# Kernel tuning notes

Hardware: AMD Instinct MI355X
Metric: run time of the kernel (lower is better)

Reference implementation:

```python
import jax, jax.numpy as jnp
import numpy as np

B, S, D, H = 4, 1024, 1024, 16
DH = D // H  # head dim = 64
NEG = 1e9  # keras Softmax masking constant for fp32


def setup_inputs() -> dict:
    key = jax.random.key(0)
    ks = jax.random.split(key, 7)
    return {
        "inputs": jax.random.normal(ks[0], (B, S, D), jnp.float32),
        "mask": jax.random.randint(ks[1], (B, 1, 1, S), 0, 2) > 0,
        "interaction": jax.random.normal(ks[2], (B, S, S, H), jnp.float32) * 0.1,
        "W_Q": jax.random.normal(ks[3], (D, D), jnp.float32) * 0.02,
        "W_K": jax.random.normal(ks[4], (D, D), jnp.float32) * 0.02,
        "W_V": jax.random.normal(ks[5], (D, D), jnp.float32) * 0.02,
        "W_O": jax.random.normal(ks[6], (D, D), jnp.float32) * 0.02,
    }


def reference(inputs, mask, interaction, W_Q, W_K, W_V, W_O):
    b, s, d = inputs.shape
    def proj(W):
        # [B,S,D] @ [D,D] -> [B,S,H,DH] -> [B,H,S,DH]
        return (inputs @ W).reshape(b, s, H, DH).transpose(0, 2, 1, 3)
    Q, K, V = proj(W_Q), proj(W_K), proj(W_V)
    scores = jnp.einsum("bhqd,bhkd->bhqk", Q, K) / (DH ** 0.5)
    # interaction [B,S,S,H] -> [B,H,S,S], additive bias before softmax
    scores = scores + interaction.transpose(0, 3, 1, 2)
    # keras Softmax(mask=...): add -1e9 where mask is False, softmax over last axis
    scores = jnp.where(mask, scores, scores - NEG)
    attn = jax.nn.softmax(scores, axis=-1)
    hidden = jnp.einsum("bhqk,bhkd->bhqd", attn, V)
    hidden = hidden.transpose(0, 2, 1, 3).reshape(b, s, d)
    return hidden @ W_O
```

## Files before the change

### kernel.cpp

```cpp
#include <hip/hip_runtime.h>
#include <hip/hip_bf16.h>
#include <stdint.h>

#define BDIM 4
#define SDIM 1024
#define DDIM 1024
#define HDIM 16
#define DHDIM 64

typedef __bf16 bf16_t;
typedef __bf16 bf16x8 __attribute__((ext_vector_type(8)));
typedef __bf16 bf16x4 __attribute__((ext_vector_type(4)));
typedef float f32x4 __attribute__((ext_vector_type(4)));

typedef __attribute__((address_space(3))) uint32_t lds_u32;
typedef const __attribute__((address_space(1))) uint32_t glb_u32;

__device__ __forceinline__ void glds16(const void* g, void* l) {
    __builtin_amdgcn_global_load_lds((glb_u32*)g, (lds_u32*)l, 16, 0, 0);
}


__global__ __launch_bounds__(256) void convert_x_kernel(const float* __restrict__ X,
                                                        bf16_t* __restrict__ Xb, int n) {
    int i = (blockIdx.x * 256 + threadIdx.x) * 4;
    if (i >= n) return;
    float4 v = *(const float4*)(X + i);
    bf16x4 o;
    o[0] = (bf16_t)v.x; o[1] = (bf16_t)v.y; o[2] = (bf16_t)v.z; o[3] = (bf16_t)v.w;
    *(bf16x4*)(Xb + i) = o;
}

__global__ __launch_bounds__(256) void transpose_w_kernel(const float* __restrict__ W0,
                                                          const float* __restrict__ W1,
                                                          const float* __restrict__ W2,
                                                          const float* __restrict__ W3,
                                                          bf16_t* __restrict__ Wt) {
    __shared__ float tile[32][33];
    int z = blockIdx.z;
    const float* W = (z == 0) ? W0 : (z == 1) ? W1 : (z == 2) ? W2 : W3;
    bf16_t* dst = Wt + (size_t)z * DDIM * DDIM;
    int bx = blockIdx.x * 32;
    int by = blockIdx.y * 32;
    int x = threadIdx.x & 31, y0 = threadIdx.x >> 5;
#pragma unroll
    for (int i = 0; i < 4; i++) {
        int y = y0 + i * 8;
        tile[y][x] = W[(size_t)(by + y) * DDIM + bx + x];
    }
    __syncthreads();
#pragma unroll
    for (int i = 0; i < 4; i++) {
        int y = y0 + i * 8;
        dst[(size_t)(bx + y) * DDIM + by + x] = (bf16_t)tile[x][y];
    }
}

__global__ __launch_bounds__(1024) void mask_flag_kernel(const unsigned char* __restrict__ mb,
                                                         int* __restrict__ flag) {
    __shared__ int any;
    if (threadIdx.x == 0) any = 0;
    __syncthreads();
    int loc = 0;
    for (int i = threadIdx.x; i < BDIM * SDIM; i += 1024)
        if ((i & 3) && mb[i]) loc = 1;
    if (loc) any = 1;
    __syncthreads();
    if (threadIdx.x == 0) *flag = any ? 1 : 0;
}

template <int MODE>
__global__ __launch_bounds__(256) void gemm_bt_kernel(const bf16_t* __restrict__ A,
                                                      const bf16_t* __restrict__ Bt,
                                                      bf16_t* __restrict__ Qo, bf16_t* __restrict__ Ko,
                                                      bf16_t* __restrict__ Vto, float* __restrict__ Co) {
    __shared__ bf16_t As[128 * 32];
    __shared__ bf16_t Bs[128 * 32];
    const int m0 = blockIdx.x * 128;
    const int n0 = blockIdx.y * 128;
    const int t = threadIdx.x;
    const int lane = t & 63, w = t >> 6;
    const int wm = w & 1, wn = w >> 1;
    const int low = lane & 15, quad = lane >> 4;
    f32x4 acc[4][4] = {};

    const int srow = w * 16 + (lane >> 2);
    const int koff = (lane & 3) * 8;
    const bf16_t* Ag = A + (size_t)(m0 + srow) * DDIM + koff;
    const bf16_t* Bg = Bt + (size_t)(n0 + srow) * DDIM + koff;
    bf16_t* AsW = As + w * 512;
    bf16_t* BsW = Bs + w * 512;

    for (int k0 = 0; k0 < DDIM; k0 += 32) {
        __syncthreads();
        glds16(Ag + k0, AsW);
        glds16(Ag + (size_t)64 * DDIM + k0, AsW + 64 * 32);
        glds16(Bg + k0, BsW);
        glds16(Bg + (size_t)64 * DDIM + k0, BsW + 64 * 32);
        __syncthreads();
        bf16x8 af[4], bv[4];
#pragma unroll
        for (int mt = 0; mt < 4; mt++)
            af[mt] = *(const bf16x8*)(As + (wm * 64 + mt * 16 + low) * 32 + quad * 8);
#pragma unroll
        for (int nt = 0; nt < 4; nt++)
            bv[nt] = *(const bf16x8*)(Bs + (wn * 64 + nt * 16 + low) * 32 + quad * 8);
#pragma unroll
        for (int mt = 0; mt < 4; mt++)
#pragma unroll
            for (int nt = 0; nt < 4; nt++)
                acc[mt][nt] = __builtin_amdgcn_mfma_f32_16x16x32_bf16(af[mt], bv[nt], acc[mt][nt], 0, 0, 0);
    }

#pragma unroll
    for (int mt = 0; mt < 4; mt++) {
#pragma unroll
        for (int nt = 0; nt < 4; nt++) {
#pragma unroll
            for (int r = 0; r < 4; r++) {
                int mrow = m0 + wm * 64 + mt * 16 + quad * 4 + r;
                int ncol = n0 + wn * 64 + nt * 16 + low;
                float vv = acc[mt][nt][r];
                if (MODE == 0) {
                    int which = ncol >> 10, nl = ncol & 1023;
                    int h = nl >> 6, dh = nl & 63;
                    int b = mrow >> 10, s = mrow & 1023;
                    if (which == 0)
                        Qo[((size_t)(b * HDIM + h) * SDIM + s) * DHDIM + dh] = (bf16_t)(vv * 0.125f);
                    else if (which == 1)
                        Ko[((size_t)(b * HDIM + h) * SDIM + s) * DHDIM + dh] = (bf16_t)vv;
                    else
                        Vto[((size_t)(b * HDIM + h) * DHDIM + dh) * SDIM + s] = (bf16_t)vv;
                } else {
                    Co[(size_t)mrow * DDIM + ncol] = vv;
                }
            }
        }
    }
}

__global__ __launch_bounds__(512) void attn_kernel(const bf16_t* __restrict__ Q,
                                                   const bf16_t* __restrict__ K,
                                                   const bf16_t* __restrict__ Vt,
                                                   const float* __restrict__ inter,
                                                   const unsigned char* __restrict__ maskb,
                                                   const int* __restrict__ flagp,
                                                   bf16_t* __restrict__ hid) {
    constexpr int KS = 20;
    constexpr int HS = 64 * KS + 4;
    __shared__ bf16_t bias_l[16 * HS];
    __shared__ float pen_l[SDIM];
    __shared__ bf16_t P[8][16 * 72];
    const int b = blockIdx.y;
    const int q0 = blockIdx.x * 16;
    const int t = threadIdx.x;
    const int w = t >> 6, lane = t & 63;
    const int low = lane & 15, quad = lane >> 4;
    const int h0 = w * 2;
    const int mstride = (*flagp) ? 1 : 4;

    for (int k = t; k < SDIM; k += 512)
        pen_l[k] = maskb[((size_t)b * SDIM + k) * mstride] ? 0.f : 1.0e9f;

    bf16x8 qf[2][2];
#pragma unroll
    for (int hh = 0; hh < 2; hh++) {
        const bf16_t* Qb = Q + ((size_t)(b * HDIM + h0 + hh) * SDIM + q0) * DHDIM;
        qf[hh][0] = *(const bf16x8*)(Qb + low * DHDIM + quad * 8);
        qf[hh][1] = *(const bf16x8*)(Qb + low * DHDIM + 32 + quad * 8);
    }

    const int sq = t >> 5;
    const int so = (t & 31) * 4;
    const int hb = (t & 3) * 4;
    const int kb = (t & 31) >> 2;
    const float* srcQ = inter + ((size_t)(b * SDIM + q0 + sq) * SDIM) * HDIM + so;

    float4 regs[8];
#pragma unroll
    for (int i = 0; i < 8; i++) regs[i] = *(const float4*)(srcQ + i * 128);

    float mrow[2][4], lrow[2][4];
    f32x4 accO[2][4] = {};
#pragma unroll
    for (int hh = 0; hh < 2; hh++)
#pragma unroll
        for (int r = 0; r < 4; r++) { mrow[hh][r] = -3.0e38f; lrow[hh][r] = 0.f; }

    __syncthreads();

    for (int c = 0; c < SDIM / 64; c++) {
#pragma unroll
        for (int i = 0; i < 8; i++) {
            int kl = kb + i * 8;
            float p = pen_l[c * 64 + kl];
            float4 v = regs[i];
            bf16_t* d = bias_l + kl * KS + sq;
            d[(hb + 0) * HS] = (bf16_t)(v.x - p);
            d[(hb + 1) * HS] = (bf16_t)(v.y - p);
            d[(hb + 2) * HS] = (bf16_t)(v.z - p);
            d[(hb + 3) * HS] = (bf16_t)(v.w - p);
        }
        __syncthreads();
        if (c + 1 < SDIM / 64) {
#pragma unroll
            for (int i = 0; i < 8; i++)
                regs[i] = *(const float4*)(srcQ + (c + 1) * 1024 + i * 128);
        }
        const int kbase = c * 64;
#pragma unroll
        for (int hh = 0; hh < 2; hh++) {
            const int h = h0 + hh;
            const bf16_t* Kb = K + (size_t)(b * HDIM + h) * SDIM * DHDIM;
            const bf16_t* VtB = Vt + (size_t)(b * HDIM + h) * DHDIM * SDIM;
            f32x4 sacc[4];
#pragma unroll
            for (int nt = 0; nt < 4; nt++) {
                const bf16_t* kp = Kb + (size_t)(kbase + nt * 16 + low) * DHDIM;
                bf16x8 kf0 = *(const bf16x8*)(kp + quad * 8);
                bf16x8 kf1 = *(const bf16x8*)(kp + 32 + quad * 8);
                f32x4 z = {};
                z = __builtin_amdgcn_mfma_f32_16x16x32_bf16(qf[hh][0], kf0, z, 0, 0, 0);
                z = __builtin_amdgcn_mfma_f32_16x16x32_bf16(qf[hh][1], kf1, z, 0, 0, 0);
                sacc[nt] = z;
            }
            float sv[4][4];
#pragma unroll
            for (int nt = 0; nt < 4; nt++) {
                bf16x4 bv = *(const bf16x4*)(bias_l + h * HS + (nt * 16 + low) * KS + quad * 4);
#pragma unroll
                for (int r = 0; r < 4; r++) sv[nt][r] = sacc[nt][r] + (float)bv[r];
            }
#pragma unroll
            for (int r = 0; r < 4; r++) {
                float vmx = fmaxf(fmaxf(sv[0][r], sv[1][r]), fmaxf(sv[2][r], sv[3][r]));
                vmx = fmaxf(vmx, __shfl_xor(vmx, 1));
                vmx = fmaxf(vmx, __shfl_xor(vmx, 2));
                vmx = fmaxf(vmx, __shfl_xor(vmx, 4));
                vmx = fmaxf(vmx, __shfl_xor(vmx, 8));
                float mn = fmaxf(mrow[hh][r], vmx);
                float alpha = __expf(mrow[hh][r] - mn);
                mrow[hh][r] = mn;
                lrow[hh][r] *= alpha;
#pragma unroll
                for (int nt = 0; nt < 4; nt++) accO[hh][nt][r] *= alpha;
                float rs = 0.f;
#pragma unroll
                for (int nt = 0; nt < 4; nt++) {
                    float p = __expf(sv[nt][r] - mn);
                    sv[nt][r] = p;
                    rs += p;
                }
                rs += __shfl_xor(rs, 1);
                rs += __shfl_xor(rs, 2);
                rs += __shfl_xor(rs, 4);
                rs += __shfl_xor(rs, 8);
                lrow[hh][r] += rs;
            }
            bf16_t* Pw = &P[w][0];
#pragma unroll
            for (int nt = 0; nt < 4; nt++)
#pragma unroll
                for (int r = 0; r < 4; r++)
                    Pw[(quad * 4 + r) * 72 + nt * 16 + low] = (bf16_t)sv[nt][r];
#pragma unroll
            for (int step = 0; step < 2; step++) {
                bf16x8 pf = *(const bf16x8*)(Pw + low * 72 + step * 32 + quad * 8);
#pragma unroll
                for (int nt = 0; nt < 4; nt++) {
                    bf16x8 vf = *(const bf16x8*)(VtB + (size_t)(nt * 16 + low) * SDIM +
                                                 kbase + step * 32 + quad * 8);
                    accO[hh][nt] = __builtin_amdgcn_mfma_f32_16x16x32_bf16(pf, vf, accO[hh][nt], 0, 0, 0);
                }
            }
        }
        __syncthreads();
    }
#pragma unroll
    for (int hh = 0; hh < 2; hh++) {
#pragma unroll
        for (int r = 0; r < 4; r++) {
            float inv = 1.f / lrow[hh][r];
#pragma unroll
            for (int nt = 0; nt < 4; nt++) {
                hid[((size_t)b * SDIM + q0 + quad * 4 + r) * DDIM + (h0 + hh) * 64 + nt * 16 + low] =
                    (bf16_t)(accO[hh][nt][r] * inv);
            }
        }
    }
}


extern "C" void kernel_launch(void* const* d_in, const int* in_sizes, int n_in,
                              void* d_out, int out_size, void* d_ws, size_t ws_size,
                              hipStream_t stream) {
    const float* X = (const float*)d_in[0];
    const unsigned char* maskb = (const unsigned char*)d_in[1];
    const float* inter = (const float*)d_in[2];
    const float* WQ = (const float*)d_in[3];
    const float* WK = (const float*)d_in[4];
    const float* WV = (const float*)d_in[5];
    const float* WO = (const float*)d_in[6];
    float* out = (float*)d_out;

    char* ws = (char*)d_ws;
    const size_t MB = 1024 * 1024;
    bf16_t* Xb  = (bf16_t*)(ws + 0 * MB);
    bf16_t* Wt  = (bf16_t*)(ws + 8 * MB);
    bf16_t* Qm  = (bf16_t*)(ws + 16 * MB);
    bf16_t* Km  = (bf16_t*)(ws + 24 * MB);
    bf16_t* Vtm = (bf16_t*)(ws + 32 * MB);
    bf16_t* hid = (bf16_t*)(ws + 40 * MB);
    int* flag   = (int*)(ws + 48 * MB);

    convert_x_kernel<<<BDIM * SDIM * DDIM / (256 * 4), 256, 0, stream>>>(X, Xb, BDIM * SDIM * DDIM);
    transpose_w_kernel<<<dim3(32, 32, 4), 256, 0, stream>>>(WQ, WK, WV, WO, Wt);
    mask_flag_kernel<<<1, 1024, 0, stream>>>(maskb, flag);
    gemm_bt_kernel<0><<<dim3(32, 24), 256, 0, stream>>>(Xb, Wt, Qm, Km, Vtm, nullptr);
    attn_kernel<<<dim3(SDIM / 16, BDIM), 512, 0, stream>>>(Qm, Km, Vtm, inter, maskb, flag, hid);
    gemm_bt_kernel<1><<<dim3(32, 8), 256, 0, stream>>>(hid, Wt + (size_t)3 * DDIM * DDIM,
                                                       nullptr, nullptr, nullptr, out);
}
```

Baseline: 639.2 us.

## Use one wave per head with 32-key chunks and double-buffered bias in attention

The attention kernel goes from 512 to 1024 threads, so each of 16 waves handles a single head instead of two. The key chunk shrinks from 64 to 32, and the interaction bias plus mask penalty is written into a double-buffered LDS tile. The next chunk's bias is loaded and stored after the current chunk's MFMAs, which drops one barrier per iteration and overlaps the bias staging with compute. The mask penalty is now read straight from global memory per chunk instead of from a precomputed LDS array, and launch bounds of (1024,4) may constrain registers.

New measurement: 565.5 us. -11.5%, faster.

```diff
diff --git a/kernel.cpp b/kernel.cpp
--- a/kernel.cpp
+++ b/kernel.cpp
@@ -139,153 +139,139 @@
     }
 }
 
-__global__ __launch_bounds__(512) void attn_kernel(const bf16_t* __restrict__ Q,
-                                                   const bf16_t* __restrict__ K,
-                                                   const bf16_t* __restrict__ Vt,
-                                                   const float* __restrict__ inter,
-                                                   const unsigned char* __restrict__ maskb,
-                                                   const int* __restrict__ flagp,
-                                                   bf16_t* __restrict__ hid) {
+__global__ __launch_bounds__(1024, 4) void attn_kernel(const bf16_t* __restrict__ Q,
+                                                       const bf16_t* __restrict__ K,
+                                                       const bf16_t* __restrict__ Vt,
+                                                       const float* __restrict__ inter,
+                                                       const unsigned char* __restrict__ maskb,
+                                                       const int* __restrict__ flagp,
+                                                       bf16_t* __restrict__ hid) {
     constexpr int KS = 20;
-    constexpr int HS = 64 * KS + 4;
-    __shared__ bf16_t bias_l[16 * HS];
-    __shared__ float pen_l[SDIM];
-    __shared__ bf16_t P[8][16 * 72];
+    constexpr int HS = 32 * KS + 4;
+    __shared__ bf16_t bias_l[2][16 * HS];
+    __shared__ bf16_t P[16][16 * 40];
     const int b = blockIdx.y;
     const int q0 = blockIdx.x * 16;
     const int t = threadIdx.x;
     const int w = t >> 6, lane = t & 63;
     const int low = lane & 15, quad = lane >> 4;
-    const int h0 = w * 2;
+    const int h = w;
     const int mstride = (*flagp) ? 1 : 4;
 
-    for (int k = t; k < SDIM; k += 512)
-        pen_l[k] = maskb[((size_t)b * SDIM + k) * mstride] ? 0.f : 1.0e9f;
-
-    bf16x8 qf[2][2];
-#pragma unroll
-    for (int hh = 0; hh < 2; hh++) {
-        const bf16_t* Qb = Q + ((size_t)(b * HDIM + h0 + hh) * SDIM + q0) * DHDIM;
-        qf[hh][0] = *(const bf16x8*)(Qb + low * DHDIM + quad * 8);
-        qf[hh][1] = *(const bf16x8*)(Qb + low * DHDIM + 32 + quad * 8);
-    }
-
-    const int sq = t >> 5;
-    const int so = (t & 31) * 4;
-    const int hb = (t & 3) * 4;
-    const int kb = (t & 31) >> 2;
-    const float* srcQ = inter + ((size_t)(b * SDIM + q0 + sq) * SDIM) * HDIM + so;
-
-    float4 regs[8];
-#pragma unroll
-    for (int i = 0; i < 8; i++) regs[i] = *(const float4*)(srcQ + i * 128);
-
-    float mrow[2][4], lrow[2][4];
-    f32x4 accO[2][4] = {};
-#pragma unroll
-    for (int hh = 0; hh < 2; hh++)
-#pragma unroll
-        for (int r = 0; r < 4; r++) { mrow[hh][r] = -3.0e38f; lrow[hh][r] = 0.f; }
-
-    __syncthreads();
-
-    for (int c = 0; c < SDIM / 64; c++) {
-#pragma unroll
-        for (int i = 0; i < 8; i++) {
-            int kl = kb + i * 8;
-            float p = pen_l[c * 64 + kl];
-            float4 v = regs[i];
-            bf16_t* d = bias_l + kl * KS + sq;
-            d[(hb + 0) * HS] = (bf16_t)(v.x - p);
-            d[(hb + 1) * HS] = (bf16_t)(v.y - p);
-            d[(hb + 2) * HS] = (bf16_t)(v.z - p);
-            d[(hb + 3) * HS] = (bf16_t)(v.w - p);
-        }
+    const int kl = lane >> 1;
+    const int hb = (lane & 1) * 8;
+    const float* srcQ = inter + ((size_t)(b * SDIM + q0 + w) * SDIM) * HDIM + lane * 8;
+    const unsigned char* mb = maskb + (size_t)b * SDIM * mstride;
+
+    const bf16_t* Qb = Q + ((size_t)(b * HDIM + h) * SDIM + q0) * DHDIM;
+    bf16x8 qf0 = *(const bf16x8*)(Qb + low * DHDIM + quad * 8);
+    bf16x8 qf1 = *(const bf16x8*)(Qb + low * DHDIM + 32 + quad * 8);
+
+    const bf16_t* Kb = K + (size_t)(b * HDIM + h) * SDIM * DHDIM;
+    const bf16_t* VtB = Vt + (size_t)(b * HDIM + h) * DHDIM * SDIM;
+    bf16_t* Pw = &P[w][0];
+
+    float mrow[4], lrow[4];
+    f32x4 accO[4] = {};
+#pragma unroll
+    for (int r = 0; r < 4; r++) { mrow[r] = -3.0e38f; lrow[r] = 0.f; }
+
+    float4 r0 = *(const float4*)(srcQ + 0);
+    float4 r1 = *(const float4*)(srcQ + 4);
+    float pcur = mb[kl * mstride] ? 0.f : 1.0e9f;
+    {
+        bf16_t* d = &bias_l[0][kl * KS + w];
+        d[(hb + 0) * HS] = (bf16_t)(r0.x - pcur);
+        d[(hb + 1) * HS] = (bf16_t)(r0.y - pcur);
+        d[(hb + 2) * HS] = (bf16_t)(r0.z - pcur);
+        d[(hb + 3) * HS] = (bf16_t)(r0.w - pcur);
+        d[(hb + 4) * HS] = (bf16_t)(r1.x - pcur);
+        d[(hb + 5) * HS] = (bf16_t)(r1.y - pcur);
+        d[(hb + 6) * HS] = (bf16_t)(r1.z - pcur);
+        d[(hb + 7) * HS] = (bf16_t)(r1.w - pcur);
+    }
+
+    for (int c = 0; c < SDIM / 32; c++) {
         __syncthreads();
-        if (c + 1 < SDIM / 64) {
-#pragma unroll
-            for (int i = 0; i < 8; i++)
-                regs[i] = *(const float4*)(srcQ + (c + 1) * 1024 + i * 128);
-        }
-        const int kbase = c * 64;
-#pragma unroll
-        for (int hh = 0; hh < 2; hh++) {
-            const int h = h0 + hh;
-            const bf16_t* Kb = K + (size_t)(b * HDIM + h) * SDIM * DHDIM;
-            const bf16_t* VtB = Vt + (size_t)(b * HDIM + h) * DHDIM * SDIM;
-            f32x4 sacc[4];
-#pragma unroll
-            for (int nt = 0; nt < 4; nt++) {
-                const bf16_t* kp = Kb + (size_t)(kbase + nt * 16 + low) * DHDIM;
-                bf16x8 kf0 = *(const bf16x8*)(kp + quad * 8);
-                bf16x8 kf1 = *(const bf16x8*)(kp + 32 + quad * 8);
-                f32x4 z = {};
-                z = __builtin_amdgcn_mfma_f32_16x16x32_bf16(qf[hh][0], kf0, z, 0, 0, 0);
-                z = __builtin_amdgcn_mfma_f32_16x16x32_bf16(qf[hh][1], kf1, z, 0, 0, 0);
-                sacc[nt] = z;
-            }
-            float sv[4][4];
-#pragma unroll
-            for (int nt = 0; nt < 4; nt++) {
-                bf16x4 bv = *(const bf16x4*)(bias_l + h * HS + (nt * 16 + low) * KS + quad * 4);
-#pragma unroll
-                for (int r = 0; r < 4; r++) sv[nt][r] = sacc[nt][r] + (float)bv[r];
-            }
-#pragma unroll
-            for (int r = 0; r < 4; r++) {
-                float vmx = fmaxf(fmaxf(sv[0][r], sv[1][r]), fmaxf(sv[2][r], sv[3][r]));
-                vmx = fmaxf(vmx, __shfl_xor(vmx, 1));
-                vmx = fmaxf(vmx, __shfl_xor(vmx, 2));
-                vmx = fmaxf(vmx, __shfl_xor(vmx, 4));
-                vmx = fmaxf(vmx, __shfl_xor(vmx, 8));
-                float mn = fmaxf(mrow[hh][r], vmx);
-                float alpha = __expf(mrow[hh][r] - mn);
-                mrow[hh][r] = mn;
-                lrow[hh][r] *= alpha;
-#pragma unroll
-                for (int nt = 0; nt < 4; nt++) accO[hh][nt][r] *= alpha;
-                float rs = 0.f;
-#pragma unroll
-                for (int nt = 0; nt < 4; nt++) {
-                    float p = __expf(sv[nt][r] - mn);
-                    sv[nt][r] = p;
-                    rs += p;
-                }
-                rs += __shfl_xor(rs, 1);
-                rs += __shfl_xor(rs, 2);
-                rs += __shfl_xor(rs, 4);
-                rs += __shfl_xor(rs, 8);
-                lrow[hh][r] += rs;
-            }
-            bf16_t* Pw = &P[w][0];
-#pragma unroll
-            for (int nt = 0; nt < 4; nt++)
-#pragma unroll
-                for (int r = 0; r < 4; r++)
-                    Pw[(quad * 4 + r) * 72 + nt * 16 + low] = (bf16_t)sv[nt][r];
-#pragma unroll
-            for (int step = 0; step < 2; step++) {
-                bf16x8 pf = *(const bf16x8*)(Pw + low * 72 + step * 32 + quad * 8);
-#pragma unroll
-                for (int nt = 0; nt < 4; nt++) {
-                    bf16x8 vf = *(const bf16x8*)(VtB + (size_t)(nt * 16 + low) * SDIM +
-                                                 kbase + step * 32 + quad * 8);
-                    accO[hh][nt] = __builtin_amdgcn_mfma_f32_16x16x32_bf16(pf, vf, accO[hh][nt], 0, 0, 0);
-                }
-            }
-        }
-        __syncthreads();
-    }
-#pragma unroll
-    for (int hh = 0; hh < 2; hh++) {
+        const int kbase = c * 32;
+        float4 n0v, n1v; float pnext = 0.f;
+        if (c + 1 < SDIM / 32) {
+            n0v = *(const float4*)(srcQ + (c + 1) * 512 + 0);
+            n1v = *(const float4*)(srcQ + (c + 1) * 512 + 4);
+            pnext = mb[((c + 1) * 32 + kl) * mstride] ? 0.f : 1.0e9f;
+        }
+        f32x4 sacc[2];
+#pragma unroll
+        for (int nt = 0; nt < 2; nt++) {
+            const bf16_t* kp = Kb + (size_t)(kbase + nt * 16 + low) * DHDIM;
+            bf16x8 kf0 = *(const bf16x8*)(kp + quad * 8);
+            bf16x8 kf1 = *(const bf16x8*)(kp + 32 + quad * 8);
+            f32x4 z = {};
+            z = __builtin_amdgcn_mfma_f32_16x16x32_bf16(qf0, kf0, z, 0, 0, 0);
+            z = __builtin_amdgcn_mfma_f32_16x16x32_bf16(qf1, kf1, z, 0, 0, 0);
+            sacc[nt] = z;
+        }
+        const bf16_t* bias_c = &bias_l[c & 1][h * HS];
+        float sv[2][4];
+#pragma unroll
+        for (int nt = 0; nt < 2; nt++) {
+            bf16x4 bv = *(const bf16x4*)(bias_c + (nt * 16 + low) * KS + quad * 4);
+#pragma unroll
+            for (int r = 0; r < 4; r++) sv[nt][r] = sacc[nt][r] + (float)bv[r];
+        }
 #pragma unroll
         for (int r = 0; r < 4; r++) {
-            float inv = 1.f / lrow[hh][r];
-#pragma unroll
-            for (int nt = 0; nt < 4; nt++) {
-                hid[((size_t)b * SDIM + q0 + quad * 4 + r) * DDIM + (h0 + hh) * 64 + nt * 16 + low] =
-                    (bf16_t)(accO[hh][nt][r] * inv);
-            }
+            float vmx = fmaxf(sv[0][r], sv[1][r]);
+            vmx = fmaxf(vmx, __shfl_xor(vmx, 1));
+            vmx = fmaxf(vmx, __shfl_xor(vmx, 2));
+            vmx = fmaxf(vmx, __shfl_xor(vmx, 4));
+            vmx = fmaxf(vmx, __shfl_xor(vmx, 8));
+            float mn = fmaxf(mrow[r], vmx);
+            float alpha = __expf(mrow[r] - mn);
+            mrow[r] = mn;
+            lrow[r] *= alpha;
+#pragma unroll
+            for (int nt = 0; nt < 4; nt++) accO[nt][r] *= alpha;
+            float p0 = __expf(sv[0][r] - mn);
+            float p1 = __expf(sv[1][r] - mn);
+            sv[0][r] = p0; sv[1][r] = p1;
+            float rs = p0 + p1;
+            rs += __shfl_xor(rs, 1);
+            rs += __shfl_xor(rs, 2);
+            rs += __shfl_xor(rs, 4);
+            rs += __shfl_xor(rs, 8);
+            lrow[r] += rs;
+        }
+#pragma unroll
+        for (int nt = 0; nt < 2; nt++)
+#pragma unroll
+            for (int r = 0; r < 4; r++)
+                Pw[(quad * 4 + r) * 40 + nt * 16 + low] = (bf16_t)sv[nt][r];
+        bf16x8 pf = *(const bf16x8*)(Pw + low * 40 + quad * 8);
+#pragma unroll
+        for (int nt = 0; nt < 4; nt++) {
+            bf16x8 vf = *(const bf16x8*)(VtB + (size_t)(nt * 16 + low) * SDIM + kbase + quad * 8);
+            accO[nt] = __builtin_amdgcn_mfma_f32_16x16x32_bf16(pf, vf, accO[nt], 0, 0, 0);
+        }
+        if (c + 1 < SDIM / 32) {
+            bf16_t* d = &bias_l[(c + 1) & 1][kl * KS + w];
+            d[(hb + 0) * HS] = (bf16_t)(n0v.x - pnext);
+            d[(hb + 1) * HS] = (bf16_t)(n0v.y - pnext);
+            d[(hb + 2) * HS] = (bf16_t)(n0v.z - pnext);
+            d[(hb + 3) * HS] = (bf16_t)(n0v.w - pnext);
+            d[(hb + 4) * HS] = (bf16_t)(n1v.x - pnext);
+            d[(hb + 5) * HS] = (bf16_t)(n1v.y - pnext);
+            d[(hb + 6) * HS] = (bf16_t)(n1v.z - pnext);
+            d[(hb + 7) * HS] = (bf16_t)(n1v.w - pnext);
+        }
+    }
+#pragma unroll
+    for (int r = 0; r < 4; r++) {
+        float inv = 1.f / lrow[r];
+#pragma unroll
+        for (int nt = 0; nt < 4; nt++) {
+            hid[((size_t)b * SDIM + q0 + quad * 4 + r) * DDIM + h * 64 + nt * 16 + low] =
+                (bf16_t)(accO[nt][r] * inv);
         }
     }
 }
@@ -317,7 +303,7 @@
     transpose_w_kernel<<<dim3(32, 32, 4), 256, 0, stream>>>(WQ, WK, WV, WO, Wt);
     mask_flag_kernel<<<1, 1024, 0, stream>>>(maskb, flag);
     gemm_bt_kernel<0><<<dim3(32, 24), 256, 0, stream>>>(Xb, Wt, Qm, Km, Vtm, nullptr);
-    attn_kernel<<<dim3(SDIM / 16, BDIM), 512, 0, stream>>>(Qm, Km, Vtm, inter, maskb, flag, hid);
+    attn_kernel<<<dim3(SDIM / 16, BDIM), 1024, 0, stream>>>(Qm, Km, Vtm, inter, maskb, flag, hid);
     gemm_bt_kernel<1><<<dim3(32, 8), 256, 0, stream>>>(hid, Wt + (size_t)3 * DDIM * DDIM,
                                                        nullptr, nullptr, nullptr, out);
 }
```
